# Optimization experiments

Measured on AMD Instinct MI355X. Metric: run time of the kernel, lower is better.

The kernel has to match this reference:

```python
import jax, jax.numpy as jnp
import numpy as np
from jax import lax

BN_EPS = 1e-5

def dwconv(x, w, dilation):
    # x: [N,C,H,W], w: [C,1,k,k] depthwise; SAME padding = (r*(k-1)+1)//2
    k = w.shape[-1]
    pad = (dilation * (k - 1) + 1) // 2
    return lax.conv_general_dilated(
        x, w, window_strides=(1, 1), padding=[(pad, pad), (pad, pad)],
        rhs_dilation=(dilation, dilation), feature_group_count=x.shape[1],
        dimension_numbers=('NCHW', 'OIHW', 'NCHW'))

def bn_eval(y, gamma, beta, mean, var):
    # inference BatchNorm2d over channel dim; params: [C]
    inv = gamma * lax.rsqrt(var + BN_EPS)
    return y * inv[None, :, None, None] + (beta - mean * inv)[None, :, None, None]

def setup_inputs() -> dict:
    key = jax.random.key(0)
    ks = jax.random.split(key, 13)
    C = 384
    x = jax.random.normal(ks[0], (16, C, 56, 56), jnp.float32)
    w_lk = jax.random.normal(ks[1], (C, 1, 13, 13), jnp.float32) * 0.05
    w_b0 = jax.random.normal(ks[2], (C, 1, 5, 5), jnp.float32) * 0.05
    w_b1 = jax.random.normal(ks[3], (C, 1, 7, 7), jnp.float32) * 0.05
    w_b2 = jax.random.normal(ks[4], (C, 1, 7, 7), jnp.float32) * 0.05
    w_b3 = jax.random.normal(ks[5], (C, 1, 3, 3), jnp.float32) * 0.05
    w_b4 = jax.random.normal(ks[6], (C, 1, 3, 3), jnp.float32) * 0.05
    w_b5 = jax.random.normal(ks[7], (C, 1, 3, 3), jnp.float32) * 0.05
    bn_gamma = jax.random.uniform(ks[8], (7, C), jnp.float32, 0.5, 1.5)
    bn_beta = jax.random.normal(ks[9], (7, C), jnp.float32) * 0.1
    bn_mean = jax.random.normal(ks[10], (7, C), jnp.float32) * 0.1
    bn_var = jax.random.uniform(ks[11], (7, C), jnp.float32, 0.5, 1.5)
    return dict(x=x, w_lk=w_lk, w_b0=w_b0, w_b1=w_b1, w_b2=w_b2, w_b3=w_b3,
                w_b4=w_b4, w_b5=w_b5, bn_gamma=bn_gamma, bn_beta=bn_beta,
                bn_mean=bn_mean, bn_var=bn_var)

def reference(x, w_lk, w_b0, w_b1, w_b2, w_b3, w_b4, w_b5,
              bn_gamma, bn_beta, bn_mean, bn_var):
    # DilatedReparamBlock (kernel_size=13, non-deploy):
    # out = BN(dw13(x)) + sum_i BN_i(dw_{k_i, r_i}(x))
    dilates = (1, 1, 2, 3, 4, 5)
    branch_ws = (w_b0, w_b1, w_b2, w_b3, w_b4, w_b5)
    out = bn_eval(dwconv(x, w_lk, 1), bn_gamma[0], bn_beta[0], bn_mean[0], bn_var[0])
    for i, (w, r) in enumerate(zip(branch_ws, dilates)):
        j = i + 1
        out = out + bn_eval(dwconv(x, w, r), bn_gamma[j], bn_beta[j], bn_mean[j], bn_var[j])
    return out
```

## Files before the change

### kernel.cpp

```cpp
#include <hip/hip_runtime.h>


#define CCH 384
#define SP 56
#define PW 68
#define NPLANES (16*384)

__device__ __forceinline__ float rfl(float v) {
    return __int_as_float(__builtin_amdgcn_readfirstlane(__float_as_int(v)));
}

__global__ __launch_bounds__(64, 2) void drb_conv13_r7(
    const float* __restrict__ x,
    const float* __restrict__ w_lk, const float* __restrict__ w_b0,
    const float* __restrict__ w_b1, const float* __restrict__ w_b2,
    const float* __restrict__ w_b3, const float* __restrict__ w_b4,
    const float* __restrict__ w_b5,
    const float* __restrict__ gamma, const float* __restrict__ beta,
    const float* __restrict__ mean, const float* __restrict__ var,
    float* __restrict__ out)
{
    __shared__ __align__(16) float sx[PW * PW];
    __shared__ __align__(16) float sw[13 * 16];

    const int plane = blockIdx.x;
    const int c = plane % CCH;
    const int tid = threadIdx.x;
    const float* __restrict__ xp = x + (size_t)plane * (SP * SP);

    float4 stage[13];
    #pragma unroll
    for (int k = 0; k < 13; k++) {
        int i4 = tid + 64 * k;
        if (i4 < SP * SP / 4) stage[k] = ((const float4*)xp)[i4];
    }

    float S[7];
    float bias = 0.f;
    #pragma unroll
    for (int j = 0; j < 7; j++) {
        float inv = gamma[j * CCH + c] * rsqrtf(var[j * CCH + c] + 1e-5f);
        S[j] = inv;
        bias += beta[j * CCH + c] - mean[j * CCH + c] * inv;
    }

    {
        float4 z = make_float4(0.f, 0.f, 0.f, 0.f);
        #pragma unroll
        for (int k = 0; k < 19; k++) {
            int i = tid + 64 * k;
            if (i < PW * PW / 4) ((float4*)sx)[i] = z;
        }
    }

    #pragma unroll
    for (int k = 0; k < 4; k++) {
        int t = tid + 64 * k;
        if (t < 13 * 16) {
            int ky = t >> 4, kx = t & 15;
            float w = 0.f;
            if (kx < 13) {
                w = S[0] * w_lk[c * 169 + ky * 13 + kx];
                if (ky >= 4 && ky <= 8 && kx >= 4 && kx <= 8)
                    w += S[1] * w_b0[c * 25 + (ky - 4) * 5 + (kx - 4)];
                if (ky >= 3 && ky <= 9 && kx >= 3 && kx <= 9)
                    w += S[2] * w_b1[c * 49 + (ky - 3) * 7 + (kx - 3)];
                if (!(ky & 1) && !(kx & 1))
                    w += S[3] * w_b2[c * 49 + (ky >> 1) * 7 + (kx >> 1)];
                if (ky >= 3 && ky <= 9 && (ky - 3) % 3 == 0 &&
                    kx >= 3 && kx <= 9 && (kx - 3) % 3 == 0)
                    w += S[4] * w_b3[c * 9 + ((ky - 3) / 3) * 3 + (kx - 3) / 3];
                if (ky >= 2 && ky <= 10 && (ky - 2) % 4 == 0 &&
                    kx >= 2 && kx <= 10 && (kx - 2) % 4 == 0)
                    w += S[5] * w_b4[c * 9 + ((ky - 2) / 4) * 3 + (kx - 2) / 4];
                if (ky >= 1 && ky <= 11 && (ky - 1) % 5 == 0 &&
                    kx >= 1 && kx <= 11 && (kx - 1) % 5 == 0)
                    w += S[6] * w_b5[c * 9 + ((ky - 1) / 5) * 3 + (kx - 1) / 5];
            }
            sw[t] = w;
        }
    }

    #pragma unroll
    for (int k = 0; k < 13; k++) {
        int i4 = tid + 64 * k;
        if (i4 < SP * SP / 4) {
            int r = i4 / 14;
            int col = (i4 - r * 14) * 4;
            float* d = &sx[(r + 6) * PW + col + 6];
            ((float2*)d)[0] = make_float2(stage[k].x, stage[k].y);
            ((float2*)d)[1] = make_float2(stage[k].z, stage[k].w);
        }
    }
    __syncthreads();

    const int xg = tid & 7;
    const int yg = tid >> 3;
    const int xgc = (xg < 7) ? xg : 3;
    const int Yb = yg * 7;
    const float* __restrict__ sbase = &sx[Yb * PW + 8 * xgc];

    float acc[7][8];
    #pragma unroll
    for (int r = 0; r < 7; r++)
        #pragma unroll
        for (int j = 0; j < 8; j++) acc[r][j] = 0.f;

    #pragma unroll 1
    for (int k0 = 0; k0 < 12; k0 += 4) {
        float w[4][13];
        #pragma unroll
        for (int dy = 0; dy < 4; dy++) {
            const float* wr = &sw[(k0 + dy) * 16];
            #pragma unroll
            for (int q = 0; q < 3; q++) {
                float4 t = ((const float4*)wr)[q];
                w[dy][4*q+0] = rfl(t.x); w[dy][4*q+1] = rfl(t.y);
                w[dy][4*q+2] = rfl(t.z); w[dy][4*q+3] = rfl(t.w);
            }
            w[dy][12] = rfl(wr[12]);
        }
        const float* sr = sbase + k0 * PW;
        #pragma unroll
        for (int i = 0; i < 10; i++) {
            float4 win4[5];
            #pragma unroll
            for (int q = 0; q < 5; q++)
                win4[q] = *(const float4*)(sr + i * PW + 4 * q);
            const float* win = (const float*)win4;
            #pragma unroll
            for (int dy = 0; dy < 4; dy++) {
                const int r = i - dy;
                if (r >= 0 && r < 7) {
                    #pragma unroll
                    for (int kx = 0; kx < 13; kx++) {
                        const float wv = w[dy][kx];
                        #pragma unroll
                        for (int j = 0; j < 8; j++)
                            acc[r][j] = fmaf(wv, win[kx + j], acc[r][j]);
                    }
                }
            }
        }
    }
    {
        float w12[13];
        const float* wr = &sw[12 * 16];
        #pragma unroll
        for (int q = 0; q < 3; q++) {
            float4 t = ((const float4*)wr)[q];
            w12[4*q+0] = rfl(t.x); w12[4*q+1] = rfl(t.y);
            w12[4*q+2] = rfl(t.z); w12[4*q+3] = rfl(t.w);
        }
        w12[12] = rfl(wr[12]);
        const float* sr = sbase + 12 * PW;
        #pragma unroll
        for (int i = 0; i < 7; i++) {
            float4 win4[5];
            #pragma unroll
            for (int q = 0; q < 5; q++)
                win4[q] = *(const float4*)(sr + i * PW + 4 * q);
            const float* win = (const float*)win4;
            #pragma unroll
            for (int kx = 0; kx < 13; kx++) {
                const float wv = w12[kx];
                #pragma unroll
                for (int j = 0; j < 8; j++)
                    acc[i][j] = fmaf(wv, win[kx + j], acc[i][j]);
            }
        }
    }

    if (xg < 7) {
        float* op = out + (size_t)plane * (SP * SP) + Yb * SP + 8 * xg;
        #pragma unroll
        for (int r = 0; r < 7; r++) {
            float4 v0 = make_float4(acc[r][0] + bias, acc[r][1] + bias,
                                    acc[r][2] + bias, acc[r][3] + bias);
            float4 v1 = make_float4(acc[r][4] + bias, acc[r][5] + bias,
                                    acc[r][6] + bias, acc[r][7] + bias);
            *(float4*)(op + r * SP) = v0;
            *(float4*)(op + r * SP + 4) = v1;
        }
    }
}

extern "C" void kernel_launch(void* const* d_in, const int* in_sizes, int n_in,
                              void* d_out, int out_size, void* d_ws, size_t ws_size,
                              hipStream_t stream) {
    const float* x    = (const float*)d_in[0];
    const float* w_lk = (const float*)d_in[1];
    const float* w_b0 = (const float*)d_in[2];
    const float* w_b1 = (const float*)d_in[3];
    const float* w_b2 = (const float*)d_in[4];
    const float* w_b3 = (const float*)d_in[5];
    const float* w_b4 = (const float*)d_in[6];
    const float* w_b5 = (const float*)d_in[7];
    const float* bn_g = (const float*)d_in[8];
    const float* bn_b = (const float*)d_in[9];
    const float* bn_m = (const float*)d_in[10];
    const float* bn_v = (const float*)d_in[11];
    float* out = (float*)d_out;

    drb_conv13_r7<<<dim3(NPLANES), dim3(64), 0, stream>>>(
        x, w_lk, w_b0, w_b1, w_b2, w_b3, w_b4, w_b5,
        bn_g, bn_b, bn_m, bn_v, out);
}
```

Measured before the change: 227.1 us.

## Split the 13-row kernel into 7+6 weight passes to reuse LDS windows

Replaces the three 4-row weight chunks plus a final row with two passes that hold 7 and then 6 kernel rows of weights in registers. This cuts the number of shared-memory window row loads per thread (from 37 to 25). It also drops the readfirstlane broadcast, so the weights sit in VGPRs instead of SGPRs. The cost is much higher VGPR pressure and a larger fully unrolled body, which could cause spills or lower occupancy.

```diff
diff --git a/kernel.cpp b/kernel.cpp
--- a/kernel.cpp
+++ b/kernel.cpp
@@ -6,11 +6,7 @@
 #define PW 68
 #define NPLANES (16*384)
 
-__device__ __forceinline__ float rfl(float v) {
-    return __int_as_float(__builtin_amdgcn_readfirstlane(__float_as_int(v)));
-}
-
-__global__ __launch_bounds__(64, 2) void drb_conv13_r7(
+__global__ __launch_bounds__(64, 2) void drb_conv13_r8(
     const float* __restrict__ x,
     const float* __restrict__ w_lk, const float* __restrict__ w_b0,
     const float* __restrict__ w_b1, const float* __restrict__ w_b2,
@@ -106,35 +102,33 @@
         #pragma unroll
         for (int j = 0; j < 8; j++) acc[r][j] = 0.f;
 
-    #pragma unroll 1
-    for (int k0 = 0; k0 < 12; k0 += 4) {
-        float w[4][13];
-        #pragma unroll
-        for (int dy = 0; dy < 4; dy++) {
-            const float* wr = &sw[(k0 + dy) * 16];
+    {
+        float wA[7][13];
+        #pragma unroll
+        for (int dy = 0; dy < 7; dy++) {
+            const float* wr = &sw[dy * 16];
             #pragma unroll
             for (int q = 0; q < 3; q++) {
                 float4 t = ((const float4*)wr)[q];
-                w[dy][4*q+0] = rfl(t.x); w[dy][4*q+1] = rfl(t.y);
-                w[dy][4*q+2] = rfl(t.z); w[dy][4*q+3] = rfl(t.w);
-            }
-            w[dy][12] = rfl(wr[12]);
-        }
-        const float* sr = sbase + k0 * PW;
-        #pragma unroll
-        for (int i = 0; i < 10; i++) {
+                wA[dy][4*q+0] = t.x; wA[dy][4*q+1] = t.y;
+                wA[dy][4*q+2] = t.z; wA[dy][4*q+3] = t.w;
+            }
+            wA[dy][12] = wr[12];
+        }
+        #pragma unroll
+        for (int i = 0; i < 13; i++) {
             float4 win4[5];
             #pragma unroll
             for (int q = 0; q < 5; q++)
-                win4[q] = *(const float4*)(sr + i * PW + 4 * q);
+                win4[q] = *(const float4*)(sbase + i * PW + 4 * q);
             const float* win = (const float*)win4;
             #pragma unroll
-            for (int dy = 0; dy < 4; dy++) {
+            for (int dy = 0; dy < 7; dy++) {
                 const int r = i - dy;
                 if (r >= 0 && r < 7) {
                     #pragma unroll
                     for (int kx = 0; kx < 13; kx++) {
-                        const float wv = w[dy][kx];
+                        const float wv = wA[dy][kx];
                         #pragma unroll
                         for (int j = 0; j < 8; j++)
                             acc[r][j] = fmaf(wv, win[kx + j], acc[r][j]);
@@ -143,30 +137,39 @@
             }
         }
     }
+
     {
-        float w12[13];
-        const float* wr = &sw[12 * 16];
-        #pragma unroll
-        for (int q = 0; q < 3; q++) {
-            float4 t = ((const float4*)wr)[q];
-            w12[4*q+0] = rfl(t.x); w12[4*q+1] = rfl(t.y);
-            w12[4*q+2] = rfl(t.z); w12[4*q+3] = rfl(t.w);
-        }
-        w12[12] = rfl(wr[12]);
-        const float* sr = sbase + 12 * PW;
-        #pragma unroll
-        for (int i = 0; i < 7; i++) {
+        float wB[6][13];
+        #pragma unroll
+        for (int dy = 0; dy < 6; dy++) {
+            const float* wr = &sw[(7 + dy) * 16];
+            #pragma unroll
+            for (int q = 0; q < 3; q++) {
+                float4 t = ((const float4*)wr)[q];
+                wB[dy][4*q+0] = t.x; wB[dy][4*q+1] = t.y;
+                wB[dy][4*q+2] = t.z; wB[dy][4*q+3] = t.w;
+            }
+            wB[dy][12] = wr[12];
+        }
+        #pragma unroll
+        for (int i = 7; i < 19; i++) {
             float4 win4[5];
             #pragma unroll
             for (int q = 0; q < 5; q++)
-                win4[q] = *(const float4*)(sr + i * PW + 4 * q);
+                win4[q] = *(const float4*)(sbase + i * PW + 4 * q);
             const float* win = (const float*)win4;
             #pragma unroll
-            for (int kx = 0; kx < 13; kx++) {
-                const float wv = w12[kx];
-                #pragma unroll
-                for (int j = 0; j < 8; j++)
-                    acc[i][j] = fmaf(wv, win[kx + j], acc[i][j]);
+            for (int dy = 0; dy < 6; dy++) {
+                const int r = i - 7 - dy;
+                if (r >= 0 && r < 7) {
+                    #pragma unroll
+                    for (int kx = 0; kx < 13; kx++) {
+                        const float wv = wB[dy][kx];
+                        #pragma unroll
+                        for (int j = 0; j < 8; j++)
+                            acc[r][j] = fmaf(wv, win[kx + j], acc[r][j]);
+                    }
+                }
             }
         }
     }
@@ -202,7 +205,7 @@
     const float* bn_v = (const float*)d_in[11];
     float* out = (float*)d_out;
 
-    drb_conv13_r7<<<dim3(NPLANES), dim3(64), 0, stream>>>(
+    drb_conv13_r8<<<dim3(NPLANES), dim3(64), 0, stream>>>(
         x, w_lk, w_b0, w_b1, w_b2, w_b3, w_b4, w_b5,
         bn_g, bn_b, bn_m, bn_v, out);
 }
```

Result: slower. 269.8 us (+18.8%).
